# Kernel tuning notes

Hardware: AMD Instinct MI355X
Metric: run time of the kernel (lower is better)

The kernel has to match this reference:

```python
import jax, jax.numpy as jnp
import numpy as np
from jax import lax

B, N, C = 8, 8192, 64
NPOINT, NSAMPLE, RADIUS = 2048, 32, 0.2
EPS = 1e-5


def setup_inputs() -> dict:
    key = jax.random.key(0)
    ks = jax.random.split(key, 14)
    xyz = jax.random.uniform(ks[0], (B, 3, N), dtype=jnp.float32)
    points = jax.random.normal(ks[1], (B, C, N), dtype=jnp.float32)
    dims = [(67, 64), (64, 64), (64, 128)]
    inp = {"xyz": xyz, "points": points}
    for i, (cin, cout) in enumerate(dims, start=1):
        inp[f"W{i}"] = jax.random.normal(ks[2 * i], (cout, cin), dtype=jnp.float32) / np.sqrt(cin)
        inp[f"b{i}"] = jnp.zeros((cout,), jnp.float32)
        inp[f"g{i}"] = jnp.ones((cout,), jnp.float32)
        inp[f"be{i}"] = jnp.zeros((cout,), jnp.float32)
    return inp


def farthest_point_sample(x, npoint):
    # x: [B, N, 3] -> [B, npoint] int32 indices
    b, n, _ = x.shape
    barange = jnp.arange(b)

    def step(carry, _):
        dist, far = carry
        centroid = x[barange, far]                      # [B, 3]
        d = jnp.sum((x - centroid[:, None, :]) ** 2, -1)  # [B, N]
        dist = jnp.minimum(dist, d)
        return (dist, jnp.argmax(dist, -1)), far

    init = (jnp.full((b, n), 1e10, x.dtype), jnp.zeros((b,), jnp.int32))
    _, cents = lax.scan(step, init, None, length=npoint)
    return cents.T  # [B, npoint]


def square_distance(src, dst):
    # src: [B, S, 3], dst: [B, D, 3] -> [B, S, D]
    d = -2.0 * jnp.einsum('bsc,bdc->bsd', src, dst)
    d += jnp.sum(src ** 2, -1)[:, :, None]
    d += jnp.sum(dst ** 2, -1)[:, None, :]
    return d


def query_ball_point(radius, nsample, x, new_x):
    b, n, _ = x.shape
    sqr = square_distance(new_x, x)                    # [B, NP, N]
    idx = jnp.where(sqr > radius ** 2, n, jnp.arange(n)[None, None, :])
    idx = jnp.sort(idx, axis=-1)[:, :, :nsample]       # [B, NP, NS]
    first = idx[:, :, :1]
    return jnp.where(idx == n, first, idx)


def _bn_relu(x, g, be):
    # x: [B, NP, NS, Cout]; batchnorm over (B, NP, NS) per channel (training stats)
    m = x.mean((0, 1, 2))
    v = x.var((0, 1, 2))
    return jax.nn.relu((x - m) * lax.rsqrt(v + EPS) * g + be)


def reference(xyz, points, W1, b1, g1, be1, W2, b2, g2, be2, W3, b3, g3, be3):
    x = xyz.transpose(0, 2, 1)       # [B, N, 3]
    p = points.transpose(0, 2, 1)    # [B, N, C]
    bidx = jnp.arange(B)[:, None, None]

    fps_idx = farthest_point_sample(x, NPOINT)               # [B, NP]
    new_xyz = jnp.take_along_axis(x, fps_idx[:, :, None], 1)  # [B, NP, 3]
    idx = query_ball_point(RADIUS, NSAMPLE, x, new_xyz)       # [B, NP, NS]

    grouped_xyz = x[bidx, idx]                                # [B, NP, NS, 3]
    grouped_norm = grouped_xyz - new_xyz[:, :, None, :]
    grouped_p = p[bidx, idx]                                  # [B, NP, NS, C]
    feat = jnp.concatenate([grouped_norm, grouped_p], -1)     # [B, NP, NS, 3+C]

    for W, b, g, be in ((W1, b1, g1, be1), (W2, b2, g2, be2), (W3, b3, g3, be3)):
        feat = _bn_relu(jnp.einsum('bpsc,oc->bpso', feat, W) + b, g, be)

    new_points = jnp.max(feat, axis=2)                        # [B, NP, Cout]
    return new_xyz.transpose(0, 2, 1), new_points.transpose(0, 2, 1)
```

## Files before the change

### kernel.cpp

```cpp
#include <hip/hip_runtime.h>
#include <hip/hip_bf16.h>
#include <stdint.h>

#define NB 8
#define NPTS 8192
#define NCH 64
#define NPOINT 2048
#define NSAMPLE 32
#define R2 0.04f

#define DPP_MAX_STEP(C) { \
  int lo2_ = __builtin_amdgcn_update_dpp(0, (int)(unsigned int)key, (C), 0xf, 0xf, true); \
  int hi2_ = __builtin_amdgcn_update_dpp(0, (int)(unsigned int)(key>>32), (C), 0xf, 0xf, true); \
  unsigned long long k2_ = ((unsigned long long)(unsigned int)hi2_ << 32) | (unsigned int)lo2_; \
  if (k2_ > key) key = k2_; }

__global__ __launch_bounds__(512) void fps_kernel(const float* __restrict__ xyz,
                                                  float* __restrict__ out)
{
  const int t = threadIdx.x;
  const int wv = t >> 6, lane = t & 63;
  const int b = blockIdx.x;
  const float* xb = xyz + (size_t)b*3*NPTS;
  __shared__ float s_px[NPTS], s_py[NPTS], s_pz[NPTS];
  __shared__ float s_ox[NPOINT], s_oy[NPOINT], s_oz[NPOINT];
  __shared__ unsigned long long s_key[2][8];
  for (int e=t; e<NPTS; e+=512){
    s_px[e]=xb[e]; s_py[e]=xb[NPTS+e]; s_pz[e]=xb[2*NPTS+e];
  }
  float px[16], py[16], pz[16], dist[16];
  const int base = (wv<<10) + lane;
  #pragma unroll
  for (int k=0;k<16;k++){
    int i = base + (k<<6);
    px[k]=xb[i]; py[k]=xb[NPTS+i]; pz[k]=xb[2*NPTS+i];
    dist[k]=1e10f;
  }
  __syncthreads();
  float cx = s_px[0], cy = s_py[0], cz = s_pz[0];
  for (int s=0;s<NPOINT;s++){
    if (t==0){ s_ox[s]=cx; s_oy[s]=cy; s_oz[s]=cz; }
    float best = -1.0f; int bidx = 0;
    #pragma unroll
    for (int k=0;k<16;k++){
      float dx=__fsub_rn(px[k],cx), dy=__fsub_rn(py[k],cy), dz=__fsub_rn(pz[k],cz);
      float d = __fadd_rn(__fadd_rn(__fmul_rn(dx,dx),__fmul_rn(dy,dy)),__fmul_rn(dz,dz));
      float nd = d < dist[k] ? d : dist[k];
      dist[k]=nd;
      if (nd > best){ best = nd; bidx = base + (k<<6); }
    }
    unsigned long long key = ((unsigned long long)__float_as_uint(best) << 13)
                           | (unsigned long long)(8191 - bidx);
    DPP_MAX_STEP(0x111)
    DPP_MAX_STEP(0x112)
    DPP_MAX_STEP(0x114)
    DPP_MAX_STEP(0x118)
    DPP_MAX_STEP(0x142)
    DPP_MAX_STEP(0x143)
    if (lane==63) s_key[s&1][wv] = key;
    __syncthreads();
    const unsigned long long* kr = s_key[s&1];
    unsigned long long k0=kr[0],k1=kr[1],k2=kr[2],k3=kr[3],
                       k4=kr[4],k5=kr[5],k6=kr[6],k7=kr[7];
    unsigned long long m01=k0>k1?k0:k1, m23=k2>k3?k2:k3;
    unsigned long long m45=k4>k5?k4:k5, m67=k6>k7?k6:k7;
    unsigned long long m03=m01>m23?m01:m23, m47=m45>m67?m45:m67;
    unsigned long long mk = m03>m47?m03:m47;
    const int far = 8191 - (int)(mk & 8191ull);
    cx = s_px[far]; cy = s_py[far]; cz = s_pz[far];
  }
  __syncthreads();
  float* oxb = out + (size_t)b*3*NPOINT;
  for (int e=t; e<NPOINT; e+=512){
    oxb[e]          = s_ox[e];
    oxb[NPOINT+e]   = s_oy[e];
    oxb[2*NPOINT+e] = s_oz[e];
  }
}

__global__ __launch_bounds__(256) void transpose_kernel(const float* __restrict__ points,
                                                        float* __restrict__ pt)
{
  __shared__ float tile[64][65];
  const int t = threadIdx.x;
  const int b  = blockIdx.x >> 7;
  const int n0 = (blockIdx.x & 127) << 6;
  const int tx = t & 63, ty = t >> 6;
  #pragma unroll
  for (int r=0; r<16; r++){
    const int c = ty*16 + r;
    tile[c][tx] = points[(size_t)b*NCH*NPTS + (size_t)c*NPTS + n0 + tx];
  }
  __syncthreads();
  #pragma unroll
  for (int r=0; r<16; r++){
    const int n = ty*16 + r;
    pt[((size_t)b*NPTS + n0 + n)*64 + tx] = tile[tx][n];
  }
}

__global__ __launch_bounds__(128) void ballmlp1_kernel(
    const float* __restrict__ xyz, const float* __restrict__ pt,
    const float* __restrict__ nxyz,
    const float* __restrict__ W1, const float* __restrict__ b1,
    float* __restrict__ z, float* __restrict__ part)
{
  __shared__ float wl[67*64];
  __shared__ float spA[128], spQ[128];
  __shared__ int s_buf[4][NSAMPLE];
  __shared__ int s_cnt[4];
  __shared__ float s_ctr[4][3];
  const int t = threadIdx.x;
  const int blk = blockIdx.x;
  for (int e=t; e<67*64; e+=128){
    int o = e/67, c = e - o*67;
    wl[c*64+o] = W1[e];
  }
  const int wv = t>>6, lane = t&63;
  for (int sub=0; sub<2; sub++){
    const int gi2 = wv*2 + sub;
    const int g = blk*4 + gi2;
    const int b = g >> 11;
    const int s = g & 2047;
    const float* ob = nxyz + (size_t)b*3*NPOINT;
    const float cx = ob[s], cy = ob[NPOINT+s], cz = ob[2*NPOINT+s];
    if (lane==0){ s_ctr[gi2][0]=cx; s_ctr[gi2][1]=cy; s_ctr[gi2][2]=cz; }
    const float csum = __fadd_rn(__fadd_rn(__fmul_rn(cx,cx),__fmul_rn(cy,cy)),__fmul_rn(cz,cz));
    const float* xb = xyz + (size_t)b*3*NPTS;
    int cnt = 0;
    for (int c0=0; c0<NPTS; c0+=64){
      const int i = c0 + lane;
      float x=xb[i], y=xb[NPTS+i], zz=xb[2*NPTS+i];
      float dot  = __fmaf_rn(cz, zz, __fmaf_rn(cy, y, __fmul_rn(cx, x)));
      float dsum = __fadd_rn(__fadd_rn(__fmul_rn(x,x),__fmul_rn(y,y)),__fmul_rn(zz,zz));
      float sqr  = __fadd_rn(__fadd_rn(__fmul_rn(-2.0f,dot), csum), dsum);
      bool in = (sqr <= R2);
      unsigned long long mm = __ballot(in);
      int rank = cnt + __popcll(mm & ((1ull<<lane)-1ull));
      if (in && rank < NSAMPLE) s_buf[gi2][rank] = i;
      cnt += (int)__popcll(mm);
      if (cnt >= NSAMPLE) break;
    }
    if (lane==0) s_cnt[gi2] = cnt;
  }
  __syncthreads();
  const int gi = t>>5, lane2 = t&31;
  const int g = blk*4 + gi;
  const int b = g >> 11;
  const int cnt = s_cnt[gi];
  const int first = s_buf[gi][0];
  const int idx = (lane2 < cnt) ? s_buf[gi][lane2] : first;
  const float* xb = xyz + (size_t)b*3*NPTS;
  float f[67];
  f[0] = __fsub_rn(xb[idx],        s_ctr[gi][0]);
  f[1] = __fsub_rn(xb[NPTS+idx],   s_ctr[gi][1]);
  f[2] = __fsub_rn(xb[2*NPTS+idx], s_ctr[gi][2]);
  const float* pr = pt + ((size_t)b*NPTS + idx)*64;
  #pragma unroll
  for (int q=0;q<16;q++){
    float4 v = *(const float4*)(pr + q*4);
    f[3+q*4+0]=v.x; f[3+q*4+1]=v.y; f[3+q*4+2]=v.z; f[3+q*4+3]=v.w;
  }
  float acc[64];
  #pragma unroll
  for (int o=0;o<64;o++) acc[o]=0.0f;
  #pragma unroll
  for (int c=0;c<67;c++){
    const float fc = f[c];
    const float* wr = &wl[c*64];
    #pragma unroll
    for (int q=0;q<16;q++){
      float4 w = *(const float4*)(wr + q*4);
      acc[q*4+0] = __fmaf_rn(fc, w.x, acc[q*4+0]);
      acc[q*4+1] = __fmaf_rn(fc, w.y, acc[q*4+1]);
      acc[q*4+2] = __fmaf_rn(fc, w.z, acc[q*4+2]);
      acc[q*4+3] = __fmaf_rn(fc, w.w, acc[q*4+3]);
    }
  }
  #pragma unroll
  for (int o=0;o<64;o++) acc[o] = __fadd_rn(acc[o], b1[o]);
  float* zb = z + (size_t)blk*8192;
  #pragma unroll
  for (int c=0;c<64;c++) zb[c*128 + t] = acc[c];
  float sA=0.f, sQ=0.f;
  const int oc = t & 63;
  for (int p=0;p<2;p++){
    __syncthreads();
    if ((t>>6)==p){
      const int r = t & 63;
      #pragma unroll
      for (int j=0;j<64;j++) wl[r*65+j] = acc[j];
    }
    __syncthreads();
    const int r0 = (t>>6)*32;
    for (int r=r0; r<r0+32; r++){
      float v = wl[r*65+oc];
      sA += v; sQ = __fmaf_rn(v,v,sQ);
    }
  }
  spA[t]=sA; spQ[t]=sQ;
  __syncthreads();
  if (t<64){
    part[(size_t)blk*128 + t]      = spA[t]+spA[t+64];
    part[(size_t)blk*128 + 64 + t] = spQ[t]+spQ[t+64];
  }
}

__global__ __launch_bounds__(128) void mlp2_kernel(
    float* __restrict__ z, const float* __restrict__ ab1,
    const float* __restrict__ W2, const float* __restrict__ b2,
    float* __restrict__ part)
{
  __shared__ float wl[67*64];
  __shared__ float spA[128], spQ[128];
  __shared__ float s_ab[128];
  const int t = threadIdx.x;
  for (int e=t; e<64*64; e+=128){
    int o = e>>6, c = e&63;
    wl[c*64+o] = W2[e];
  }
  if (t<128) s_ab[t] = ab1[t];
  __syncthreads();
  float* zb = z + (size_t)blockIdx.x*8192;
  float f[64];
  #pragma unroll
  for (int c=0;c<64;c++){
    float v = zb[c*128 + t];
    float a = __fmaf_rn(v, s_ab[c], s_ab[64+c]);
    f[c] = a > 0.f ? a : 0.f;
  }
  float acc[64];
  #pragma unroll
  for (int o=0;o<64;o++) acc[o]=0.0f;
  #pragma unroll
  for (int c=0;c<64;c++){
    const float fc = f[c];
    const float* wr = &wl[c*64];
    #pragma unroll
    for (int q=0;q<16;q++){
      float4 w = *(const float4*)(wr + q*4);
      acc[q*4+0] = __fmaf_rn(fc, w.x, acc[q*4+0]);
      acc[q*4+1] = __fmaf_rn(fc, w.y, acc[q*4+1]);
      acc[q*4+2] = __fmaf_rn(fc, w.z, acc[q*4+2]);
      acc[q*4+3] = __fmaf_rn(fc, w.w, acc[q*4+3]);
    }
  }
  #pragma unroll
  for (int o=0;o<64;o++) acc[o] = __fadd_rn(acc[o], b2[o]);
  #pragma unroll
  for (int c=0;c<64;c++) zb[c*128 + t] = acc[c];
  float sA=0.f, sQ=0.f;
  const int oc = t & 63;
  for (int p=0;p<2;p++){
    __syncthreads();
    if ((t>>6)==p){
      const int r = t & 63;
      #pragma unroll
      for (int j=0;j<64;j++) wl[r*65+j] = acc[j];
    }
    __syncthreads();
    const int r0 = (t>>6)*32;
    for (int r=r0; r<r0+32; r++){
      float v = wl[r*65+oc];
      sA += v; sQ = __fmaf_rn(v,v,sQ);
    }
  }
  spA[t]=sA; spQ[t]=sQ;
  __syncthreads();
  if (t<64){
    part[(size_t)blockIdx.x*128 + t]      = spA[t]+spA[t+64];
    part[(size_t)blockIdx.x*128 + 64 + t] = spQ[t]+spQ[t+64];
  }
}

__global__ __launch_bounds__(256) void mlp3_kernel(
    const float* __restrict__ z, const float* __restrict__ ab2,
    const float* __restrict__ W3, const float* __restrict__ b3,
    float* __restrict__ gmax, float* __restrict__ part)
{
  __shared__ float wl[128*65];
  __shared__ float spA[256], spQ[256];
  __shared__ float s_ab[128];
  const int t = threadIdx.x;
  const int m0 = blockIdx.x*128;
  const int sm = t>>1, h = t&1;
  for (int e=t; e<64*128; e+=256){
    int o = e>>6, c = e&63;
    wl[c*128+o] = W3[e];
  }
  if (t<128) s_ab[t] = ab2[t];
  __syncthreads();
  const float* zb = z + (size_t)blockIdx.x*8192;
  float f[64];
  #pragma unroll
  for (int c=0;c<64;c++){
    float v = zb[c*128 + sm];
    float a = __fmaf_rn(v, s_ab[c], s_ab[64+c]);
    f[c] = a > 0.f ? a : 0.f;
  }
  float acc[64];
  #pragma unroll
  for (int o=0;o<64;o++) acc[o]=0.0f;
  #pragma unroll
  for (int c=0;c<64;c++){
    const float fc = f[c];
    const float* wr = &wl[c*128 + h*64];
    #pragma unroll
    for (int q=0;q<16;q++){
      float4 w = *(const float4*)(wr + q*4);
      acc[q*4+0] = __fmaf_rn(fc, w.x, acc[q*4+0]);
      acc[q*4+1] = __fmaf_rn(fc, w.y, acc[q*4+1]);
      acc[q*4+2] = __fmaf_rn(fc, w.z, acc[q*4+2]);
      acc[q*4+3] = __fmaf_rn(fc, w.w, acc[q*4+3]);
    }
  }
  #pragma unroll
  for (int j=0;j<64;j++) acc[j] = __fadd_rn(acc[j], b3[h*64+j]);
  for (int p=0;p<2;p++){
    __syncthreads();
    if (h==p){
      const int r = sm;
      #pragma unroll
      for (int j=0;j<64;j++) wl[r*65+j] = acc[j];
    }
    __syncthreads();
    const int oc = t & 63;
    const int q4 = t >> 6;
    float sA=0.f, sQ=0.f;
    for (int r=q4*32; r<q4*32+32; r++){
      float v = wl[r*65+oc];
      sA += v; sQ = __fmaf_rn(v,v,sQ);
    }
    spA[t]=sA; spQ[t]=sQ;
    __syncthreads();
    if (t<64){
      float A = spA[t]+spA[t+64]+spA[t+128]+spA[t+192];
      float Q = spQ[t]+spQ[t+64]+spQ[t+128]+spQ[t+192];
      part[(size_t)blockIdx.x*256 + p*64 + t]       = A;
      part[(size_t)blockIdx.x*256 + 128 + p*64 + t] = Q;
    }
  }
  #pragma unroll
  for (int off=2; off<64; off<<=1){
    #pragma unroll
    for (int j=0;j<64;j++){
      float ov = __shfl_xor(acc[j], off, 64);
      acc[j] = acc[j] > ov ? acc[j] : ov;
    }
  }
  const int lane = t & 63, w = t >> 6;
  const int gg = (m0>>5) + w;
  if (lane < 2){
    float* gp = gmax + (size_t)gg*128 + lane*64;
    #pragma unroll
    for (int q=0;q<16;q++){
      float4 v; v.x=acc[q*4]; v.y=acc[q*4+1]; v.z=acc[q*4+2]; v.w=acc[q*4+3];
      *(float4*)(gp + q*4) = v;
    }
  }
}

__global__ __launch_bounds__(64) void reduce_kernel(const float* __restrict__ part,
    const float* __restrict__ gw, const float* __restrict__ bew,
    float* __restrict__ ab, int cout, int nblk)
{
  const int o = blockIdx.x, t = threadIdx.x;
  const int stride = 2*cout;
  float A=0.f, Q=0.f;
  for (int i=t;i<nblk;i+=64){
    A += part[(size_t)i*stride + o];
    Q += part[(size_t)i*stride + cout + o];
  }
  #pragma unroll
  for (int off=1; off<64; off<<=1){
    A += __shfl_xor(A, off, 64);
    Q += __shfl_xor(Q, off, 64);
  }
  if (t==0){
    const float inv = 1.0f/524288.0f;
    float mean = A*inv;
    float var  = Q*inv - mean*mean;
    float a = gw[o] / sqrtf(var + 1e-5f);
    ab[o] = a;
    ab[cout+o] = bew[o] - mean*a;
  }
}

__global__ __launch_bounds__(256) void final_kernel(const float* __restrict__ gmax,
    const float* __restrict__ ab3, float* __restrict__ out)
{
  __shared__ float tile[32*129];
  __shared__ float s_a[128], s_b[128];
  const int t = threadIdx.x;
  const int b = blockIdx.x >> 6;
  const int s0 = (blockIdx.x & 63)*32;
  if (t<128){ s_a[t]=ab3[t]; s_b[t]=ab3[128+t]; }
  const float* gp = gmax + ((size_t)b*NPOINT + s0)*128;
  for (int e=t; e<32*32; e+=256){
    int r = e>>5, q = e&31;
    float4 v = *(const float4*)(gp + r*128 + q*4);
    tile[r*129 + q*4+0]=v.x; tile[r*129 + q*4+1]=v.y;
    tile[r*129 + q*4+2]=v.z; tile[r*129 + q*4+3]=v.w;
  }
  __syncthreads();
  float* ob = out + 49152 + (size_t)b*128*NPOINT;
  for (int e=t; e<128*32; e+=256){
    int o = e>>5, ls = e&31;
    float v = tile[ls*129 + o];
    v = __fmaf_rn(v, s_a[o], s_b[o]);
    v = v > 0.f ? v : 0.f;
    ob[(size_t)o*NPOINT + s0 + ls] = v;
  }
}

extern "C" void kernel_launch(void* const* d_in, const int* in_sizes, int n_in,
                              void* d_out, int out_size, void* d_ws, size_t ws_size,
                              hipStream_t stream)
{
  const float* xyz    = (const float*)d_in[0];
  const float* points = (const float*)d_in[1];
  const float* W1 = (const float*)d_in[2];
  const float* b1 = (const float*)d_in[3];
  const float* g1 = (const float*)d_in[4];
  const float* be1= (const float*)d_in[5];
  const float* W2 = (const float*)d_in[6];
  const float* b2 = (const float*)d_in[7];
  const float* g2 = (const float*)d_in[8];
  const float* be2= (const float*)d_in[9];
  const float* W3 = (const float*)d_in[10];
  const float* b3 = (const float*)d_in[11];
  const float* g3 = (const float*)d_in[12];
  const float* be3= (const float*)d_in[13];
  float* out = (float*)d_out;
  char* ws = (char*)d_ws;
  float* z     = (float*)(ws);
  float* pt    = (float*)(ws + 134217728);
  float* gmax  = (float*)(ws + 134217728);
  float* part3 = (float*)(ws + 142606336);
  float* part2 = (float*)(ws + 146800640);
  float* part1 = (float*)(ws + 150994944);
  float* ab1   = (float*)(ws + 153092096);
  float* ab2   = (float*)(ws + 153092608);
  float* ab3   = (float*)(ws + 153093120);

  hipLaunchKernelGGL(fps_kernel,      dim3(NB),   dim3(512), 0, stream, xyz, out);
  hipLaunchKernelGGL(transpose_kernel,dim3(1024), dim3(256), 0, stream, points, pt);
  hipLaunchKernelGGL(ballmlp1_kernel, dim3(4096), dim3(128), 0, stream, xyz, pt, out, W1, b1, z, part1);
  hipLaunchKernelGGL(reduce_kernel,   dim3(64),   dim3(64),  0, stream, part1, g1, be1, ab1, 64, 4096);
  hipLaunchKernelGGL(mlp2_kernel,     dim3(4096), dim3(128), 0, stream, z, ab1, W2, b2, part2);
  hipLaunchKernelGGL(reduce_kernel,   dim3(64),   dim3(64),  0, stream, part2, g2, be2, ab2, 64, 4096);
  hipLaunchKernelGGL(mlp3_kernel,     dim3(4096), dim3(256), 0, stream, z, ab2, W3, b3, gmax, part3);
  hipLaunchKernelGGL(reduce_kernel,   dim3(128),  dim3(64),  0, stream, part3, g3, be3, ab3, 128, 4096);
  hipLaunchKernelGGL(final_kernel,    dim3(512),  dim3(256), 0, stream, gmax, ab3, out);
}
```

Before: 2.575 ms.

## Use register-blocked 8x8 outer-product tiling for the three MLP layers

```diff
diff --git a/kernel.cpp b/kernel.cpp
--- a/kernel.cpp
+++ b/kernel.cpp
@@ -106,7 +106,7 @@
     float* __restrict__ z, float* __restrict__ part)
 {
   __shared__ float wl[67*64];
-  __shared__ float spA[128], spQ[128];
+  __shared__ float fl[67*128];
   __shared__ int s_buf[4][NSAMPLE];
   __shared__ int s_cnt[4];
   __shared__ float s_ctr[4][3];
@@ -144,65 +144,78 @@
     if (lane==0) s_cnt[gi2] = cnt;
   }
   __syncthreads();
-  const int gi = t>>5, lane2 = t&31;
-  const int g = blk*4 + gi;
-  const int b = g >> 11;
-  const int cnt = s_cnt[gi];
-  const int first = s_buf[gi][0];
-  const int idx = (lane2 < cnt) ? s_buf[gi][lane2] : first;
-  const float* xb = xyz + (size_t)b*3*NPTS;
-  float f[67];
-  f[0] = __fsub_rn(xb[idx],        s_ctr[gi][0]);
-  f[1] = __fsub_rn(xb[NPTS+idx],   s_ctr[gi][1]);
-  f[2] = __fsub_rn(xb[2*NPTS+idx], s_ctr[gi][2]);
-  const float* pr = pt + ((size_t)b*NPTS + idx)*64;
-  #pragma unroll
-  for (int q=0;q<16;q++){
-    float4 v = *(const float4*)(pr + q*4);
-    f[3+q*4+0]=v.x; f[3+q*4+1]=v.y; f[3+q*4+2]=v.z; f[3+q*4+3]=v.w;
-  }
+  {
+    const int gi = t>>5, lane2 = t&31;
+    const int g = blk*4 + gi;
+    const int b = g >> 11;
+    const int cnt = s_cnt[gi];
+    const int first = s_buf[gi][0];
+    const int idx = (lane2 < cnt) ? s_buf[gi][lane2] : first;
+    const float* xb = xyz + (size_t)b*3*NPTS;
+    fl[0*128+t] = __fsub_rn(xb[idx],        s_ctr[gi][0]);
+    fl[1*128+t] = __fsub_rn(xb[NPTS+idx],   s_ctr[gi][1]);
+    fl[2*128+t] = __fsub_rn(xb[2*NPTS+idx], s_ctr[gi][2]);
+    const float* pr = pt + ((size_t)b*NPTS + idx)*64;
+    #pragma unroll
+    for (int q=0;q<16;q++){
+      float4 v = *(const float4*)(pr + q*4);
+      fl[(3+q*4+0)*128+t]=v.x; fl[(3+q*4+1)*128+t]=v.y;
+      fl[(3+q*4+2)*128+t]=v.z; fl[(3+q*4+3)*128+t]=v.w;
+    }
+  }
+  __syncthreads();
+  const int tx = t & 15, ty = t >> 4;
   float acc[64];
   #pragma unroll
-  for (int o=0;o<64;o++) acc[o]=0.0f;
-  #pragma unroll
+  for (int i=0;i<64;i++) acc[i]=0.0f;
   for (int c=0;c<67;c++){
-    const float fc = f[c];
-    const float* wr = &wl[c*64];
-    #pragma unroll
-    for (int q=0;q<16;q++){
-      float4 w = *(const float4*)(wr + q*4);
-      acc[q*4+0] = __fmaf_rn(fc, w.x, acc[q*4+0]);
-      acc[q*4+1] = __fmaf_rn(fc, w.y, acc[q*4+1]);
-      acc[q*4+2] = __fmaf_rn(fc, w.z, acc[q*4+2]);
-      acc[q*4+3] = __fmaf_rn(fc, w.w, acc[q*4+3]);
-    }
-  }
-  #pragma unroll
-  for (int o=0;o<64;o++) acc[o] = __fadd_rn(acc[o], b1[o]);
+    float4 fa = *(const float4*)&fl[c*128 + tx*8];
+    float4 fb = *(const float4*)&fl[c*128 + tx*8 + 4];
+    float4 wa = *(const float4*)&wl[c*64 + ty*8];
+    float4 wb = *(const float4*)&wl[c*64 + ty*8 + 4];
+    float fv[8] = {fa.x,fa.y,fa.z,fa.w,fb.x,fb.y,fb.z,fb.w};
+    float wv8[8] = {wa.x,wa.y,wa.z,wa.w,wb.x,wb.y,wb.z,wb.w};
+    #pragma unroll
+    for (int oo=0;oo<8;oo++)
+      #pragma unroll
+      for (int ss=0;ss<8;ss++)
+        acc[oo*8+ss] = __fmaf_rn(fv[ss], wv8[oo], acc[oo*8+ss]);
+  }
+  #pragma unroll
+  for (int oo=0;oo<8;oo++){
+    const float bb = b1[ty*8+oo];
+    #pragma unroll
+    for (int ss=0;ss<8;ss++) acc[oo*8+ss] = __fadd_rn(acc[oo*8+ss], bb);
+  }
   float* zb = z + (size_t)blk*8192;
   #pragma unroll
-  for (int c=0;c<64;c++) zb[c*128 + t] = acc[c];
-  float sA=0.f, sQ=0.f;
-  const int oc = t & 63;
-  for (int p=0;p<2;p++){
-    __syncthreads();
-    if ((t>>6)==p){
-      const int r = t & 63;
-      #pragma unroll
-      for (int j=0;j<64;j++) wl[r*65+j] = acc[j];
-    }
-    __syncthreads();
-    const int r0 = (t>>6)*32;
-    for (int r=r0; r<r0+32; r++){
-      float v = wl[r*65+oc];
+  for (int oo=0;oo<8;oo++){
+    float4 v0; v0.x=acc[oo*8+0]; v0.y=acc[oo*8+1]; v0.z=acc[oo*8+2]; v0.w=acc[oo*8+3];
+    float4 v1; v1.x=acc[oo*8+4]; v1.y=acc[oo*8+5]; v1.z=acc[oo*8+6]; v1.w=acc[oo*8+7];
+    *(float4*)(zb + (ty*8+oo)*128 + tx*8)     = v0;
+    *(float4*)(zb + (ty*8+oo)*128 + tx*8 + 4) = v1;
+  }
+  __syncthreads();
+  float* spA = fl;
+  float* spQ = fl + 64*17;
+  #pragma unroll
+  for (int oo=0;oo<8;oo++){
+    float sA=0.f, sQ=0.f;
+    #pragma unroll
+    for (int ss=0;ss<8;ss++){
+      float v = acc[oo*8+ss];
       sA += v; sQ = __fmaf_rn(v,v,sQ);
     }
-  }
-  spA[t]=sA; spQ[t]=sQ;
-  __syncthreads();
-  if (t<64){
-    part[(size_t)blk*128 + t]      = spA[t]+spA[t+64];
-    part[(size_t)blk*128 + 64 + t] = spQ[t]+spQ[t+64];
+    spA[(ty*8+oo)*17 + tx] = sA;
+    spQ[(ty*8+oo)*17 + tx] = sQ;
+  }
+  __syncthreads();
+  if (t < 64){
+    float A=0.f, Q=0.f;
+    #pragma unroll
+    for (int j=0;j<16;j++){ A += spA[t*17+j]; Q += spQ[t*17+j]; }
+    part[(size_t)blk*128 + t]      = A;
+    part[(size_t)blk*128 + 64 + t] = Q;
   }
 }
 
@@ -211,8 +224,8 @@
     const float* __restrict__ W2, const float* __restrict__ b2,
     float* __restrict__ part)
 {
-  __shared__ float wl[67*64];
-  __shared__ float spA[128], spQ[128];
+  __shared__ float wl[64*64];
+  __shared__ float fl[64*128];
   __shared__ float s_ab[128];
   const int t = threadIdx.x;
   for (int e=t; e<64*64; e+=128){
@@ -222,54 +235,63 @@
   if (t<128) s_ab[t] = ab1[t];
   __syncthreads();
   float* zb = z + (size_t)blockIdx.x*8192;
-  float f[64];
-  #pragma unroll
   for (int c=0;c<64;c++){
     float v = zb[c*128 + t];
     float a = __fmaf_rn(v, s_ab[c], s_ab[64+c]);
-    f[c] = a > 0.f ? a : 0.f;
-  }
+    fl[c*128 + t] = a > 0.f ? a : 0.f;
+  }
+  __syncthreads();
+  const int tx = t & 15, ty = t >> 4;
   float acc[64];
   #pragma unroll
-  for (int o=0;o<64;o++) acc[o]=0.0f;
-  #pragma unroll
+  for (int i=0;i<64;i++) acc[i]=0.0f;
   for (int c=0;c<64;c++){
-    const float fc = f[c];
-    const float* wr = &wl[c*64];
-    #pragma unroll
-    for (int q=0;q<16;q++){
-      float4 w = *(const float4*)(wr + q*4);
-      acc[q*4+0] = __fmaf_rn(fc, w.x, acc[q*4+0]);
-      acc[q*4+1] = __fmaf_rn(fc, w.y, acc[q*4+1]);
-      acc[q*4+2] = __fmaf_rn(fc, w.z, acc[q*4+2]);
-      acc[q*4+3] = __fmaf_rn(fc, w.w, acc[q*4+3]);
-    }
-  }
-  #pragma unroll
-  for (int o=0;o<64;o++) acc[o] = __fadd_rn(acc[o], b2[o]);
-  #pragma unroll
-  for (int c=0;c<64;c++) zb[c*128 + t] = acc[c];
-  float sA=0.f, sQ=0.f;
-  const int oc = t & 63;
-  for (int p=0;p<2;p++){
-    __syncthreads();
-    if ((t>>6)==p){
-      const int r = t & 63;
+    float4 fa = *(const float4*)&fl[c*128 + tx*8];
+    float4 fb = *(const float4*)&fl[c*128 + tx*8 + 4];
+    float4 wa = *(const float4*)&wl[c*64 + ty*8];
+    float4 wb = *(const float4*)&wl[c*64 + ty*8 + 4];
+    float fv[8] = {fa.x,fa.y,fa.z,fa.w,fb.x,fb.y,fb.z,fb.w};
+    float wv8[8] = {wa.x,wa.y,wa.z,wa.w,wb.x,wb.y,wb.z,wb.w};
+    #pragma unroll
+    for (int oo=0;oo<8;oo++)
       #pragma unroll
-      for (int j=0;j<64;j++) wl[r*65+j] = acc[j];
-    }
-    __syncthreads();
-    const int r0 = (t>>6)*32;
-    for (int r=r0; r<r0+32; r++){
-      float v = wl[r*65+oc];
+      for (int ss=0;ss<8;ss++)
+        acc[oo*8+ss] = __fmaf_rn(fv[ss], wv8[oo], acc[oo*8+ss]);
+  }
+  #pragma unroll
+  for (int oo=0;oo<8;oo++){
+    const float bb = b2[ty*8+oo];
+    #pragma unroll
+    for (int ss=0;ss<8;ss++) acc[oo*8+ss] = __fadd_rn(acc[oo*8+ss], bb);
+  }
+  #pragma unroll
+  for (int oo=0;oo<8;oo++){
+    float4 v0; v0.x=acc[oo*8+0]; v0.y=acc[oo*8+1]; v0.z=acc[oo*8+2]; v0.w=acc[oo*8+3];
+    float4 v1; v1.x=acc[oo*8+4]; v1.y=acc[oo*8+5]; v1.z=acc[oo*8+6]; v1.w=acc[oo*8+7];
+    *(float4*)(zb + (ty*8+oo)*128 + tx*8)     = v0;
+    *(float4*)(zb + (ty*8+oo)*128 + tx*8 + 4) = v1;
+  }
+  __syncthreads();
+  float* spA = fl;
+  float* spQ = fl + 64*17;
+  #pragma unroll
+  for (int oo=0;oo<8;oo++){
+    float sA=0.f, sQ=0.f;
+    #pragma unroll
+    for (int ss=0;ss<8;ss++){
+      float v = acc[oo*8+ss];
       sA += v; sQ = __fmaf_rn(v,v,sQ);
     }
-  }
-  spA[t]=sA; spQ[t]=sQ;
-  __syncthreads();
-  if (t<64){
-    part[(size_t)blockIdx.x*128 + t]      = spA[t]+spA[t+64];
-    part[(size_t)blockIdx.x*128 + 64 + t] = spQ[t]+spQ[t+64];
+    spA[(ty*8+oo)*17 + tx] = sA;
+    spQ[(ty*8+oo)*17 + tx] = sQ;
+  }
+  __syncthreads();
+  if (t < 64){
+    float A=0.f, Q=0.f;
+    #pragma unroll
+    for (int j=0;j<16;j++){ A += spA[t*17+j]; Q += spQ[t*17+j]; }
+    part[(size_t)blockIdx.x*128 + t]      = A;
+    part[(size_t)blockIdx.x*128 + 64 + t] = Q;
   }
 }
 
@@ -278,85 +300,85 @@
     const float* __restrict__ W3, const float* __restrict__ b3,
     float* __restrict__ gmax, float* __restrict__ part)
 {
-  __shared__ float wl[128*65];
-  __shared__ float spA[256], spQ[256];
+  __shared__ float wl[64*128];
+  __shared__ float fl[64*128];
   __shared__ float s_ab[128];
   const int t = threadIdx.x;
-  const int m0 = blockIdx.x*128;
-  const int sm = t>>1, h = t&1;
+  const int blk = blockIdx.x;
   for (int e=t; e<64*128; e+=256){
     int o = e>>6, c = e&63;
     wl[c*128+o] = W3[e];
   }
   if (t<128) s_ab[t] = ab2[t];
   __syncthreads();
-  const float* zb = z + (size_t)blockIdx.x*8192;
-  float f[64];
-  #pragma unroll
+  const float* zb = z + (size_t)blk*8192;
+  for (int e=t; e<64*128; e+=256){
+    int c = e>>7, s = e&127;
+    float v = zb[c*128 + s];
+    float a = __fmaf_rn(v, s_ab[c], s_ab[64+c]);
+    fl[c*128 + s] = a > 0.f ? a : 0.f;
+  }
+  __syncthreads();
+  const int tx = t & 15, ty = t >> 4;
+  float acc[64];
+  #pragma unroll
+  for (int i=0;i<64;i++) acc[i]=0.0f;
   for (int c=0;c<64;c++){
-    float v = zb[c*128 + sm];
-    float a = __fmaf_rn(v, s_ab[c], s_ab[64+c]);
-    f[c] = a > 0.f ? a : 0.f;
-  }
-  float acc[64];
-  #pragma unroll
-  for (int o=0;o<64;o++) acc[o]=0.0f;
-  #pragma unroll
-  for (int c=0;c<64;c++){
-    const float fc = f[c];
-    const float* wr = &wl[c*128 + h*64];
-    #pragma unroll
-    for (int q=0;q<16;q++){
-      float4 w = *(const float4*)(wr + q*4);
-      acc[q*4+0] = __fmaf_rn(fc, w.x, acc[q*4+0]);
-      acc[q*4+1] = __fmaf_rn(fc, w.y, acc[q*4+1]);
-      acc[q*4+2] = __fmaf_rn(fc, w.z, acc[q*4+2]);
-      acc[q*4+3] = __fmaf_rn(fc, w.w, acc[q*4+3]);
-    }
-  }
-  #pragma unroll
-  for (int j=0;j<64;j++) acc[j] = __fadd_rn(acc[j], b3[h*64+j]);
-  for (int p=0;p<2;p++){
-    __syncthreads();
-    if (h==p){
-      const int r = sm;
+    float4 fa = *(const float4*)&fl[c*128 + tx*8];
+    float4 fb = *(const float4*)&fl[c*128 + tx*8 + 4];
+    float4 wa = *(const float4*)&wl[c*128 + ty*8];
+    float4 wb = *(const float4*)&wl[c*128 + ty*8 + 4];
+    float fv[8] = {fa.x,fa.y,fa.z,fa.w,fb.x,fb.y,fb.z,fb.w};
+    float wv8[8] = {wa.x,wa.y,wa.z,wa.w,wb.x,wb.y,wb.z,wb.w};
+    #pragma unroll
+    for (int oo=0;oo<8;oo++)
       #pragma unroll
-      for (int j=0;j<64;j++) wl[r*65+j] = acc[j];
-    }
-    __syncthreads();
-    const int oc = t & 63;
-    const int q4 = t >> 6;
-    float sA=0.f, sQ=0.f;
-    for (int r=q4*32; r<q4*32+32; r++){
-      float v = wl[r*65+oc];
+      for (int ss=0;ss<8;ss++)
+        acc[oo*8+ss] = __fmaf_rn(fv[ss], wv8[oo], acc[oo*8+ss]);
+  }
+  #pragma unroll
+  for (int oo=0;oo<8;oo++){
+    const float bb = b3[ty*8+oo];
+    #pragma unroll
+    for (int ss=0;ss<8;ss++) acc[oo*8+ss] = __fadd_rn(acc[oo*8+ss], bb);
+  }
+  __syncthreads();
+  float* spA = wl;
+  float* spQ = wl + 128*17;
+  float* sm  = fl;
+  #pragma unroll
+  for (int oo=0;oo<8;oo++){
+    float sA=0.f, sQ=0.f, mx=acc[oo*8+0];
+    #pragma unroll
+    for (int ss=0;ss<8;ss++){
+      float v = acc[oo*8+ss];
       sA += v; sQ = __fmaf_rn(v,v,sQ);
-    }
-    spA[t]=sA; spQ[t]=sQ;
-    __syncthreads();
-    if (t<64){
-      float A = spA[t]+spA[t+64]+spA[t+128]+spA[t+192];
-      float Q = spQ[t]+spQ[t+64]+spQ[t+128]+spQ[t+192];
-      part[(size_t)blockIdx.x*256 + p*64 + t]       = A;
-      part[(size_t)blockIdx.x*256 + 128 + p*64 + t] = Q;
-    }
-  }
-  #pragma unroll
-  for (int off=2; off<64; off<<=1){
-    #pragma unroll
-    for (int j=0;j<64;j++){
-      float ov = __shfl_xor(acc[j], off, 64);
-      acc[j] = acc[j] > ov ? acc[j] : ov;
-    }
-  }
-  const int lane = t & 63, w = t >> 6;
-  const int gg = (m0>>5) + w;
-  if (lane < 2){
-    float* gp = gmax + (size_t)gg*128 + lane*64;
-    #pragma unroll
-    for (int q=0;q<16;q++){
-      float4 v; v.x=acc[q*4]; v.y=acc[q*4+1]; v.z=acc[q*4+2]; v.w=acc[q*4+3];
-      *(float4*)(gp + q*4) = v;
-    }
+      mx = v > mx ? v : mx;
+    }
+    spA[(ty*8+oo)*17 + tx] = sA;
+    spQ[(ty*8+oo)*17 + tx] = sQ;
+    sm[tx*132 + ty*8+oo] = mx;
+  }
+  __syncthreads();
+  if (t < 128){
+    float A=0.f, Q=0.f;
+    #pragma unroll
+    for (int j=0;j<16;j++){ A += spA[t*17+j]; Q += spQ[t*17+j]; }
+    part[(size_t)blk*256 + t]       = A;
+    part[(size_t)blk*256 + 128 + t] = Q;
+  }
+  #pragma unroll
+  for (int r=0;r<2;r++){
+    const int id = t + r*256;
+    const int g = id >> 7, o = id & 127;
+    float m0 = sm[(g*4+0)*132 + o];
+    float m1 = sm[(g*4+1)*132 + o];
+    float m2 = sm[(g*4+2)*132 + o];
+    float m3 = sm[(g*4+3)*132 + o];
+    float mm = m0 > m1 ? m0 : m1;
+    float nn = m2 > m3 ? m2 : m3;
+    mm = mm > nn ? mm : nn;
+    gmax[((size_t)blk*4 + g)*128 + o] = mm;
   }
 }
 
```

Result: faster. 2.343 ms, median of 2 (-9.0%).
